# Performance work log

Hardware: AMD Instinct MI355X
Metric: run time of the kernel (lower is better)

## Reference

```python
import jax, jax.numpy as jnp
import numpy as np

B, N, K, F, L, H, ZMAX = 16, 1024, 16, 128, 4, 128, 100


def setup_inputs() -> dict:
    key = jax.random.key(0)
    ks = jax.random.split(key, 12)
    cell = jnp.eye(3, dtype=jnp.float32)[None] * 8.0 + 0.05 * jax.random.normal(ks[0], (B, 3, 3), dtype=jnp.float32)
    x = jax.random.uniform(ks[1], (B, N, 3), dtype=jnp.float32)
    z = jax.random.randint(ks[2], (B, N), 0, ZMAX)
    struct_size = jnp.full((B,), N, dtype=jnp.int32)
    emb = 0.02 * jax.random.normal(ks[3], (ZMAX, F), dtype=jnp.float32)
    din = 2 * F + 1
    W1 = jax.random.normal(ks[4], (L, din, F), dtype=jnp.float32) / np.sqrt(din)
    b1 = jnp.zeros((L, F), dtype=jnp.float32)
    W2 = jax.random.normal(ks[5], (L, F, F), dtype=jnp.float32) / np.sqrt(F)
    b2 = jnp.zeros((L, F), dtype=jnp.float32)
    A1 = jax.random.normal(ks[6], (din, H), dtype=jnp.float32) / np.sqrt(din)
    a1 = jnp.zeros((H,), dtype=jnp.float32)
    A2 = jax.random.normal(ks[7], (H, 1), dtype=jnp.float32) / np.sqrt(H)
    a2 = jnp.zeros((1,), dtype=jnp.float32)
    return {"cell": cell, "x": x, "z": z, "struct_size": struct_size, "emb": emb,
            "W1": W1, "b1": b1, "W2": W2, "b2": b2, "A1": A1, "a1": a1, "A2": A2, "a2": a2}


def _periodic_knn(cell, frac, k):
    # frac: [B,N,3] fractional coords, cell: [B,3,3] lattice rows.
    b, n, _ = frac.shape
    g = jnp.arange(-1, 2, dtype=frac.dtype)
    shifts = jnp.stack(jnp.meshgrid(g, g, g, indexing="ij"), -1).reshape(-1, 3)  # [27,3]
    rel = frac[:, None, :, :] - frac[:, :, None, :]  # rel[b,i,j] = frac_j - frac_i, [B,N,N,3]

    def body(carry, si):
        bd2, bsi = carry
        s, i = si
        cart = jnp.einsum("bijd,bde->bije", rel + s, cell)
        d2 = jnp.sum(cart * cart, axis=-1)
        upd = d2 < bd2
        return (jnp.where(upd, d2, bd2), jnp.where(upd, i, bsi)), None

    init = (jnp.full((b, n, n), 1e30, dtype=frac.dtype), jnp.zeros((b, n, n), dtype=jnp.int32))
    (d2min, simin), _ = jax.lax.scan(body, init, (shifts, jnp.arange(27, dtype=jnp.int32)))
    eye = jnp.eye(n, dtype=bool)
    d2min = jnp.where(eye[None], 1e30, d2min)  # exclude self (zero-shift) edges
    _, idx = jax.lax.top_k(-d2min, k)  # [B,N,k] neighbor indices
    sid = jnp.take_along_axis(simin, idx, axis=2)  # best image shift per edge
    svec = shifts[sid]  # [B,N,k,3]
    frac_j = jax.vmap(lambda f, i: f[i])(frac, idx)  # [B,N,k,3]
    vec = jnp.einsum("bnkd,bde->bnke", frac_j - frac[:, :, None, :] + svec, cell)
    d = jnp.sqrt(jnp.maximum(jnp.sum(vec * vec, axis=-1), 1e-12))  # [B,N,k]
    return idx, vec, d


def _edge_feat(h, idx, d):
    hj = jax.vmap(lambda hb, ib: hb[ib])(h, idx)  # [B,N,k,F]
    hi = jnp.broadcast_to(h[:, :, None, :], hj.shape)
    return jnp.concatenate([hi, hj, d[..., None]], axis=-1)  # [B,N,k,2F+1]


def reference(cell, x, z, struct_size, emb, W1, b1, W2, b2, A1, a1, A2, a2):
    frac = jnp.mod(x, 1.0)
    idx, vec, d = _periodic_knn(cell, frac, K)
    h = emb[z]  # [B,N,F]
    for l in range(W1.shape[0]):
        feat = _edge_feat(h, idx, d)
        m = jax.nn.silu(feat @ W1[l] + b1[l]) @ W2[l] + b2[l]  # [B,N,k,F]
        h = h + jnp.mean(m, axis=2)
    feat = _edge_feat(h, idx, d)
    w = jax.nn.silu(feat @ A1 + a1) @ A2 + a2  # [B,N,k,1]
    delta_cart = jnp.sum(w * vec, axis=2)  # [B,N,3]
    delta_frac = jnp.einsum("bnd,bde->bne", delta_cart, jnp.linalg.inv(cell))
    return x + delta_frac
```

## Files before the change

### kernel.cpp

```cpp
#include <hip/hip_runtime.h>

#define B_ 16
#define N_ 1024
#define K_ 16
#define F_ 128
#define L_ 4
#define DIN_ 257

typedef __bf16 bf16x8 __attribute__((ext_vector_type(8)));
typedef float f32x4 __attribute__((ext_vector_type(4)));

__device__ __forceinline__ float silu_f(float x) {
    return x / (1.0f + __expf(-x));
}

__device__ __forceinline__ unsigned short f2bf_bits(float f) {
    unsigned u = __builtin_bit_cast(unsigned, f);
    return (unsigned short)((u + 0x7FFFu + ((u >> 16) & 1u)) >> 16);
}

__global__ __launch_bounds__(256) void k_embed(const int* __restrict__ z,
                                               const float* __restrict__ emb,
                                               float* __restrict__ h,
                                               unsigned short* __restrict__ hbf) {
    int t = blockIdx.x * 256 + threadIdx.x;
    int node = t >> 5;
    int f4 = (t & 31) << 2;
    if (node >= B_ * N_) return;
    int zi = z[node];
    float4 v = *reinterpret_cast<const float4*>(&emb[zi * F_ + f4]);
    *reinterpret_cast<float4*>(&h[node * F_ + f4]) = v;
    ushort4 pk;
    pk.x = f2bf_bits(v.x); pk.y = f2bf_bits(v.y);
    pk.z = f2bf_bits(v.z); pk.w = f2bf_bits(v.w);
    *reinterpret_cast<ushort4*>(&hbf[node * F_ + f4]) = pk;
}

__global__ __launch_bounds__(256) void k_wconv(const float* __restrict__ W1,
                                               const float* __restrict__ W2,
                                               const float* __restrict__ A1,
                                               unsigned short* __restrict__ Wt1,
                                               unsigned short* __restrict__ Wt2,
                                               unsigned short* __restrict__ At1) {
    int id = blockIdx.x * 256 + threadIdx.x;
    if (id < L_ * 256 * 128) {
        int k = id & 127, n = (id >> 7) & 255, l = id >> 15;
        float v = (n < 128) ? W1[(size_t)l * DIN_ * F_ + (size_t)k * F_ + n]
                            : W1[(size_t)l * DIN_ * F_ + (size_t)(128 + k) * F_ + (n - 128)];
        Wt1[id] = f2bf_bits(v);
        return;
    }
    id -= L_ * 256 * 128;
    if (id < L_ * 128 * 128) {
        int k = id & 127, n = (id >> 7) & 127, l = id >> 14;
        Wt2[id] = f2bf_bits(W2[(size_t)l * F_ * F_ + (size_t)k * F_ + n]);
        return;
    }
    id -= L_ * 128 * 128;
    if (id < 256 * 128) {
        int k = id & 127, n = id >> 7;
        float v = (n < 128) ? A1[(size_t)k * 128 + n]
                            : A1[(size_t)(128 + k) * 128 + (n - 128)];
        At1[id] = f2bf_bits(v);
    }
}

__global__ __launch_bounds__(256) void k_knn(const float* __restrict__ x,
                                             const float* __restrict__ cell,
                                             int* __restrict__ idx_o,
                                             float* __restrict__ vec_o,
                                             float* __restrict__ d_o) {
    __shared__ float fr[N_ * 3];
    int b = blockIdx.x >> 8;
    int ib = (blockIdx.x & 255) << 2;
    const float* xb = x + b * N_ * 3;
    for (int u = threadIdx.x; u < N_ * 3; u += 256) {
        float xv = xb[u];
        fr[u] = xv - floorf(xv);
    }
    __syncthreads();
    int wave = threadIdx.x >> 6;
    int lane = threadIdx.x & 63;
    int i = ib + wave;

    const float* cb = cell + b * 9;
    float c00 = cb[0], c01 = cb[1], c02 = cb[2];
    float c10 = cb[3], c11 = cb[4], c12 = cb[5];
    float c20 = cb[6], c21 = cb[7], c22 = cb[8];
    float fi0 = fr[i * 3 + 0], fi1 = fr[i * 3 + 1], fi2 = fr[i * 3 + 2];

    unsigned long long k[16];
#pragma unroll
    for (int t = 0; t < 16; ++t) {
        int j = t * 64 + lane;
        float r0 = fr[j * 3 + 0] - fi0;
        float r1 = fr[j * 3 + 1] - fi1;
        float r2 = fr[j * 3 + 2] - fi2;
        float s0f = (r0 > 0.f) ? -1.f : 0.f;
        float s1f = (r1 > 0.f) ? -1.f : 0.f;
        float s2f = (r2 > 0.f) ? -1.f : 0.f;
        int sid_base = ((r0 > 0.f) ? 0 : 9) + ((r1 > 0.f) ? 0 : 3) + ((r2 > 0.f) ? 0 : 1);
        float rx0 = r0 + s0f, rx1 = r0 + (s0f + 1.0f);
        float ry0 = r1 + s1f, ry1 = r1 + (s1f + 1.0f);
        float rz0 = r2 + s2f, rz1 = r2 + (s2f + 1.0f);
        float best = 3e38f;
        int bsid = 0;
#pragma unroll
        for (int cbo = 0; cbo < 8; ++cbo) {
            float rs0 = (cbo & 4) ? rx1 : rx0;
            float rs1 = (cbo & 2) ? ry1 : ry0;
            float rs2 = (cbo & 1) ? rz1 : rz0;
            float cx = fmaf(rs2, c20, fmaf(rs1, c10, rs0 * c00));
            float cy = fmaf(rs2, c21, fmaf(rs1, c11, rs0 * c01));
            float cz = fmaf(rs2, c22, fmaf(rs1, c12, rs0 * c02));
            float d2 = fmaf(cz, cz, fmaf(cy, cy, cx * cx));
            int sid = sid_base + ((cbo >> 2) & 1) * 9 + ((cbo >> 1) & 1) * 3 + (cbo & 1);
            if (d2 < best) { best = d2; bsid = sid; }
        }
        if (j == i) best = 3e38f;
        unsigned db = __builtin_bit_cast(unsigned, best);
        k[t] = ((unsigned long long)db << 32) | (unsigned)((j << 5) | bsid);
    }

#define CE_(a, b)                                              \
    {                                                          \
        unsigned long long x_ = k[a], y_ = k[b];               \
        bool s_ = y_ < x_;                                     \
        k[a] = s_ ? y_ : x_;                                   \
        k[b] = s_ ? x_ : y_;                                   \
    }
    CE_(0,1) CE_(2,3) CE_(4,5) CE_(6,7) CE_(8,9) CE_(10,11) CE_(12,13) CE_(14,15)
    CE_(0,2) CE_(1,3) CE_(4,6) CE_(5,7) CE_(8,10) CE_(9,11) CE_(12,14) CE_(13,15)
    CE_(1,2) CE_(5,6) CE_(9,10) CE_(13,14)
    CE_(0,4) CE_(1,5) CE_(2,6) CE_(3,7) CE_(8,12) CE_(9,13) CE_(10,14) CE_(11,15)
    CE_(2,4) CE_(3,5) CE_(10,12) CE_(11,13)
    CE_(1,2) CE_(3,4) CE_(5,6) CE_(9,10) CE_(11,12) CE_(13,14)
    CE_(0,8) CE_(1,9) CE_(2,10) CE_(3,11) CE_(4,12) CE_(5,13) CE_(6,14) CE_(7,15)
    CE_(4,8) CE_(5,9) CE_(6,10) CE_(7,11)
    CE_(2,4) CE_(3,5) CE_(6,8) CE_(7,9) CE_(10,12) CE_(11,13)
    CE_(1,2) CE_(3,4) CE_(5,6) CE_(7,8) CE_(9,10) CE_(11,12) CE_(13,14)
#undef CE_

    unsigned long long sel = 0;
    for (int r = 0; r < 16; ++r) {
        unsigned long long m = k[0];
#pragma unroll
        for (int off = 32; off >= 1; off >>= 1) {
            unsigned long long o = __shfl_xor(m, off);
            if (o < m) m = o;
        }
        if (k[0] == m) {
#pragma unroll
            for (int t = 0; t < 15; ++t) k[t] = k[t + 1];
            k[15] = ~0ull;
        }
        if (lane == r) sel = m;
    }

    if (lane < 16) {
        unsigned pk = (unsigned)sel;
        int j = pk >> 5, sid = pk & 31;
        int s0 = sid / 9 - 1, s1 = (sid / 3) % 3 - 1, s2 = sid % 3 - 1;
        float rs0 = (fr[j * 3 + 0] - fi0) + (float)s0;
        float rs1 = (fr[j * 3 + 1] - fi1) + (float)s1;
        float rs2 = (fr[j * 3 + 2] - fi2) + (float)s2;
        float vx = fmaf(rs2, c20, fmaf(rs1, c10, rs0 * c00));
        float vy = fmaf(rs2, c21, fmaf(rs1, c11, rs0 * c01));
        float vz = fmaf(rs2, c22, fmaf(rs1, c12, rs0 * c02));
        float d2 = fmaf(vz, vz, fmaf(vy, vy, vx * vx));
        float dd = sqrtf(fmaxf(d2, 1e-12f));
        int node = b * N_ + i;
        int eo = node * K_ + lane;
        idx_o[eo] = j;
        d_o[eo] = dd;
        vec_o[eo * 3 + 0] = vx;
        vec_o[eo * 3 + 1] = vy;
        vec_o[eo * 3 + 2] = vz;
    }
}

template <int LOG_NT>
__global__ __launch_bounds__(256) void k_wgemm(const unsigned short* __restrict__ A,
                                               const unsigned short* __restrict__ Bt,
                                               float* __restrict__ C, int ldc) {
    constexpr int NT = 1 << LOG_NT;
    int wave = threadIdx.x >> 6, lane = threadIdx.x & 63;
    int tile = blockIdx.x * 4 + wave;
    int mt = tile >> LOG_NT, nt = tile & (NT - 1);
    int fr16 = lane & 15, ko = lane >> 4;
    const unsigned short* Ap = A + (size_t)(mt * 32 + fr16) * 128 + ko * 8;
    const unsigned short* Bp = Bt + (size_t)(nt * 32 + fr16) * 128 + ko * 8;

    bf16x8 a0[4], a1[4], b0[4], b1[4];
#pragma unroll
    for (int ks = 0; ks < 4; ++ks) {
        a0[ks] = *reinterpret_cast<const bf16x8*>(Ap + ks * 32);
        a1[ks] = *reinterpret_cast<const bf16x8*>(Ap + 16 * 128 + ks * 32);
        b0[ks] = *reinterpret_cast<const bf16x8*>(Bp + ks * 32);
        b1[ks] = *reinterpret_cast<const bf16x8*>(Bp + 16 * 128 + ks * 32);
    }
    f32x4 acc00 = {0.f, 0.f, 0.f, 0.f}, acc01 = acc00, acc10 = acc00, acc11 = acc00;
#pragma unroll
    for (int ks = 0; ks < 4; ++ks) {
        acc00 = __builtin_amdgcn_mfma_f32_16x16x32_bf16(a0[ks], b0[ks], acc00, 0, 0, 0);
        acc01 = __builtin_amdgcn_mfma_f32_16x16x32_bf16(a0[ks], b1[ks], acc01, 0, 0, 0);
        acc10 = __builtin_amdgcn_mfma_f32_16x16x32_bf16(a1[ks], b0[ks], acc10, 0, 0, 0);
        acc11 = __builtin_amdgcn_mfma_f32_16x16x32_bf16(a1[ks], b1[ks], acc11, 0, 0, 0);
    }
    int mrow = mt * 32 + ko * 4;
    int cbase = nt * 32 + fr16;
#define EPI_(FM, FN, ACC)                                                    \
    {                                                                        \
        int cc = cbase + FN * 16;                                            \
        _Pragma("unroll") for (int r = 0; r < 4; ++r) {                      \
            int row = mrow + FM * 16 + r;                                    \
            C[(size_t)row * ldc + cc] = ACC[r];                              \
        }                                                                    \
    }
    EPI_(0, 0, acc00) EPI_(0, 1, acc01) EPI_(1, 0, acc10) EPI_(1, 1, acc11)
#undef EPI_
}

__global__ __launch_bounds__(256) void k_layer(const float* __restrict__ UVin,
                                               const int* __restrict__ idx,
                                               const float* __restrict__ nd,
                                               const float* __restrict__ w1d,
                                               const float* __restrict__ b1l,
                                               const unsigned short* __restrict__ W2t,
                                               const float* __restrict__ b2l,
                                               float* __restrict__ h,
                                               const unsigned short* __restrict__ W1n,
                                               float* __restrict__ UVout) {
    __shared__ unsigned short svl[32][136];
    __shared__ unsigned short hbl[32][136];
    __shared__ int ilds[512];
    __shared__ float dlds[512];
    int tid = threadIdx.x;
    int gb = blockIdx.x;
    int batch = (gb & 7) + 8 * (gb >> 8);
    int ib = (gb >> 3) & 31;
    int node0 = batch * N_ + ib * 32;
    int bbase = batch * N_;

    ilds[tid] = idx[node0 * K_ + tid];
    ilds[tid + 256] = idx[node0 * K_ + tid + 256];
    dlds[tid] = nd[node0 * K_ + tid];
    dlds[tid + 256] = nd[node0 * K_ + tid + 256];
    __syncthreads();

#pragma unroll
    for (int it = 0; it < 2; ++it) {
        int tsk = it * 256 + tid;
        int gn = tsk >> 4, fc = tsk & 15, f0 = fc << 3;
        int node = node0 + gn;
        float u[8], wd[8], bb[8], acc[8];
#pragma unroll
        for (int q = 0; q < 8; q += 4) {
            float4 t = *reinterpret_cast<const float4*>(&UVin[(size_t)node * 256 + f0 + q]);
            u[q] = t.x; u[q + 1] = t.y; u[q + 2] = t.z; u[q + 3] = t.w;
            float4 t2 = *reinterpret_cast<const float4*>(&w1d[f0 + q]);
            wd[q] = t2.x; wd[q + 1] = t2.y; wd[q + 2] = t2.z; wd[q + 3] = t2.w;
            float4 t3 = *reinterpret_cast<const float4*>(&b1l[f0 + q]);
            bb[q] = t3.x; bb[q + 1] = t3.y; bb[q + 2] = t3.z; bb[q + 3] = t3.w;
        }
#pragma unroll
        for (int q = 0; q < 8; ++q) acc[q] = 0.f;
        for (int e = 0; e < K_; ++e) {
            int j = ilds[gn * K_ + e];
            float dd = dlds[gn * K_ + e];
            const float* vp = &UVin[(size_t)(bbase + j) * 256 + 128 + f0];
#pragma unroll
            for (int q = 0; q < 8; q += 4) {
                float4 t = *reinterpret_cast<const float4*>(&vp[q]);
                float v4[4] = {t.x, t.y, t.z, t.w};
#pragma unroll
                for (int w = 0; w < 4; ++w) {
                    float pre = u[q + w] + v4[w] + fmaf(dd, wd[q + w], bb[q + w]);
                    acc[q + w] += silu_f(pre);
                }
            }
        }
        const float inv_k = 1.0f / (float)K_;
        unsigned ow[4];
#pragma unroll
        for (int q = 0; q < 4; ++q)
            ow[q] = (unsigned)f2bf_bits(acc[2 * q] * inv_k) |
                    ((unsigned)f2bf_bits(acc[2 * q + 1] * inv_k) << 16);
        *reinterpret_cast<int4*>(&svl[gn][f0]) = make_int4(ow[0], ow[1], ow[2], ow[3]);
    }
    __syncthreads();

    int wave = tid >> 6, lane = tid & 63;
    int fr16 = lane & 15, ko = lane >> 4;

    {
        const unsigned short* Bp = W2t + (size_t)(wave * 32 + fr16) * 128 + ko * 8;
        bf16x8 a0[4], a1[4], b0[4], b1f[4];
#pragma unroll
        for (int ks = 0; ks < 4; ++ks) {
            a0[ks] = *reinterpret_cast<const bf16x8*>(&svl[fr16][ks * 32 + ko * 8]);
            a1[ks] = *reinterpret_cast<const bf16x8*>(&svl[fr16 + 16][ks * 32 + ko * 8]);
            b0[ks] = *reinterpret_cast<const bf16x8*>(Bp + ks * 32);
            b1f[ks] = *reinterpret_cast<const bf16x8*>(Bp + 16 * 128 + ks * 32);
        }
        f32x4 acc00 = {0.f, 0.f, 0.f, 0.f}, acc01 = acc00, acc10 = acc00, acc11 = acc00;
#pragma unroll
        for (int ks = 0; ks < 4; ++ks) {
            acc00 = __builtin_amdgcn_mfma_f32_16x16x32_bf16(a0[ks], b0[ks], acc00, 0, 0, 0);
            acc01 = __builtin_amdgcn_mfma_f32_16x16x32_bf16(a0[ks], b1f[ks], acc01, 0, 0, 0);
            acc10 = __builtin_amdgcn_mfma_f32_16x16x32_bf16(a1[ks], b0[ks], acc10, 0, 0, 0);
            acc11 = __builtin_amdgcn_mfma_f32_16x16x32_bf16(a1[ks], b1f[ks], acc11, 0, 0, 0);
        }
        int mrow = ko * 4;
        int cb0 = wave * 32 + fr16;
#define EPI2_(FM, FN, ACC)                                                     \
    {                                                                          \
        int col = cb0 + FN * 16;                                               \
        float bv = b2l[col];                                                   \
        _Pragma("unroll") for (int r = 0; r < 4; ++r) {                        \
            int row = mrow + FM * 16 + r;                                      \
            int grow = node0 + row;                                            \
            float val = ACC[r] + bv + h[(size_t)grow * 128 + col];             \
            h[(size_t)grow * 128 + col] = val;                                 \
            hbl[row][col] = f2bf_bits(val);                                    \
        }                                                                      \
    }
        EPI2_(0, 0, acc00) EPI2_(0, 1, acc01) EPI2_(1, 0, acc10) EPI2_(1, 1, acc11)
#undef EPI2_
    }
    __syncthreads();

#pragma unroll
    for (int half = 0; half < 2; ++half) {
        int nt = wave + half * 4;
        const unsigned short* Bp = W1n + (size_t)(nt * 32 + fr16) * 128 + ko * 8;
        bf16x8 a0[4], a1[4], b0[4], b1f[4];
#pragma unroll
        for (int ks = 0; ks < 4; ++ks) {
            a0[ks] = *reinterpret_cast<const bf16x8*>(&hbl[fr16][ks * 32 + ko * 8]);
            a1[ks] = *reinterpret_cast<const bf16x8*>(&hbl[fr16 + 16][ks * 32 + ko * 8]);
            b0[ks] = *reinterpret_cast<const bf16x8*>(Bp + ks * 32);
            b1f[ks] = *reinterpret_cast<const bf16x8*>(Bp + 16 * 128 + ks * 32);
        }
        f32x4 acc00 = {0.f, 0.f, 0.f, 0.f}, acc01 = acc00, acc10 = acc00, acc11 = acc00;
#pragma unroll
        for (int ks = 0; ks < 4; ++ks) {
            acc00 = __builtin_amdgcn_mfma_f32_16x16x32_bf16(a0[ks], b0[ks], acc00, 0, 0, 0);
            acc01 = __builtin_amdgcn_mfma_f32_16x16x32_bf16(a0[ks], b1f[ks], acc01, 0, 0, 0);
            acc10 = __builtin_amdgcn_mfma_f32_16x16x32_bf16(a1[ks], b0[ks], acc10, 0, 0, 0);
            acc11 = __builtin_amdgcn_mfma_f32_16x16x32_bf16(a1[ks], b1f[ks], acc11, 0, 0, 0);
        }
        int mrow = ko * 4;
        int cb0 = nt * 32 + fr16;
#define EPI1_(FM, FN, ACC)                                                     \
    {                                                                          \
        int col = cb0 + FN * 16;                                               \
        _Pragma("unroll") for (int r = 0; r < 4; ++r) {                        \
            int row = mrow + FM * 16 + r;                                      \
            UVout[(size_t)(node0 + row) * 256 + col] = ACC[r];                 \
        }                                                                      \
    }
        EPI1_(0, 0, acc00) EPI1_(0, 1, acc01) EPI1_(1, 0, acc10) EPI1_(1, 1, acc11)
#undef EPI1_
    }
}

__global__ __launch_bounds__(256) void k_final(const float* __restrict__ P,
                                               const int* __restrict__ idx,
                                               const float* __restrict__ nd,
                                               const float* __restrict__ nvec,
                                               const float* __restrict__ A1d,
                                               const float* __restrict__ a1v,
                                               const float* __restrict__ A2v,
                                               const float* __restrict__ a2v,
                                               const float* __restrict__ x,
                                               const float* __restrict__ cell,
                                               float* __restrict__ out) {
    __shared__ float plds[16][256];
    __shared__ float wlds[16][17];
    __shared__ float dclds[16][3];
    int gb = blockIdx.x;
    int batch = (gb & 7) + 8 * (gb >> 9);
    int ib = (gb >> 3) & 63;
    int node0 = batch * N_ + ib * 16;
    int g = threadIdx.x >> 4, fc = threadIdx.x & 15;
    int node = node0 + g;
    int b = node >> 10;
    int f0 = fc * 8;
    float pa[8], ad[8], aa[8], a2r[8];
#pragma unroll
    for (int q = 0; q < 8; q += 4) {
        float4 t = *reinterpret_cast<const float4*>(&P[(size_t)node * 256 + f0 + q]);
        pa[q] = t.x; pa[q + 1] = t.y; pa[q + 2] = t.z; pa[q + 3] = t.w;
        float4 t2 = *reinterpret_cast<const float4*>(&A1d[f0 + q]);
        ad[q] = t2.x; ad[q + 1] = t2.y; ad[q + 2] = t2.z; ad[q + 3] = t2.w;
        float4 t3 = *reinterpret_cast<const float4*>(&a1v[f0 + q]);
        aa[q] = t3.x; aa[q + 1] = t3.y; aa[q + 2] = t3.z; aa[q + 3] = t3.w;
        float4 t4 = *reinterpret_cast<const float4*>(&A2v[f0 + q]);
        a2r[q] = t4.x; a2r[q + 1] = t4.y; a2r[q + 2] = t4.z; a2r[q + 3] = t4.w;
    }
    int ebase = node * K_;
    for (int e = 0; e < K_; ++e) {
        int j = idx[ebase + e];
        float dd = nd[ebase + e];
        const float* vp = &P[(size_t)(b * N_ + j) * 256 + 128 + f0];
        float part = 0.f;
#pragma unroll
        for (int q = 0; q < 8; q += 4) {
            float4 t = *reinterpret_cast<const float4*>(&vp[q]);
            float v4[4] = {t.x, t.y, t.z, t.w};
#pragma unroll
            for (int w = 0; w < 4; ++w) {
                float pre = pa[q + w] + v4[w] + fmaf(dd, ad[q + w], aa[q + w]);
                part = fmaf(silu_f(pre), a2r[q + w], part);
            }
        }
        plds[e][(g << 4) | fc] = part;
    }
    __syncthreads();
    {
        int g2 = threadIdx.x >> 4, e2 = threadIdx.x & 15;
        float w = a2v[0];
#pragma unroll
        for (int f2 = 0; f2 < 16; ++f2) w += plds[e2][(g2 << 4) | f2];
        wlds[g2][e2] = w;
    }
    __syncthreads();
    if (threadIdx.x < 48) {
        int gg = threadIdx.x & 15, c = threadIdx.x >> 4;
        int noded = node0 + gg;
        float dc = 0.f;
#pragma unroll
        for (int e = 0; e < K_; ++e)
            dc = fmaf(wlds[gg][e], nvec[(size_t)(noded * K_ + e) * 3 + c], dc);
        dclds[gg][c] = dc;
    }
    __syncthreads();
    if (threadIdx.x < 48) {
        int gg = threadIdx.x & 15, c = threadIdx.x >> 4;
        int noded = node0 + gg;
        int bb2 = noded >> 10;
        const float* cb = cell + bb2 * 9;
        float c00 = cb[0], c01 = cb[1], c02 = cb[2];
        float c10 = cb[3], c11 = cb[4], c12 = cb[5];
        float c20 = cb[6], c21 = cb[7], c22 = cb[8];
        float det = c00 * (c11 * c22 - c12 * c21) - c01 * (c10 * c22 - c12 * c20) +
                    c02 * (c10 * c21 - c11 * c20);
        float rdet = 1.0f / det;
        float i0c, i1c, i2c;
        if (c == 0) {
            i0c = (c11 * c22 - c12 * c21) * rdet;
            i1c = -(c10 * c22 - c12 * c20) * rdet;
            i2c = (c10 * c21 - c11 * c20) * rdet;
        } else if (c == 1) {
            i0c = -(c01 * c22 - c02 * c21) * rdet;
            i1c = (c00 * c22 - c02 * c20) * rdet;
            i2c = -(c00 * c21 - c01 * c20) * rdet;
        } else {
            i0c = (c01 * c12 - c02 * c11) * rdet;
            i1c = -(c00 * c12 - c02 * c10) * rdet;
            i2c = (c00 * c11 - c01 * c10) * rdet;
        }
        float df = dclds[gg][0] * i0c + dclds[gg][1] * i1c + dclds[gg][2] * i2c;
        out[(size_t)noded * 3 + c] = x[(size_t)noded * 3 + c] + df;
    }
}

extern "C" void kernel_launch(void* const* d_in, const int* in_sizes, int n_in,
                              void* d_out, int out_size, void* d_ws, size_t ws_size,
                              hipStream_t stream) {
    (void)in_sizes; (void)n_in; (void)out_size; (void)ws_size;
    const float* cell = (const float*)d_in[0];
    const float* x    = (const float*)d_in[1];
    const int*   z    = (const int*)d_in[2];
    const float* emb  = (const float*)d_in[4];
    const float* W1   = (const float*)d_in[5];
    const float* b1   = (const float*)d_in[6];
    const float* W2   = (const float*)d_in[7];
    const float* b2   = (const float*)d_in[8];
    const float* A1   = (const float*)d_in[9];
    const float* a1   = (const float*)d_in[10];
    const float* A2   = (const float*)d_in[11];
    const float* a2   = (const float*)d_in[12];
    float* out = (float*)d_out;

    char* ws = (char*)d_ws;
    size_t off = 0;
    auto alloc = [&](size_t bytes) {
        void* p = ws + off;
        off = (off + bytes + 255) & ~(size_t)255;
        return p;
    };
    int* idx    = (int*)alloc((size_t)B_ * N_ * K_ * 4);
    float* nd   = (float*)alloc((size_t)B_ * N_ * K_ * 4);
    float* nvec = (float*)alloc((size_t)B_ * N_ * K_ * 3 * 4);
    float* h0   = (float*)alloc((size_t)B_ * N_ * F_ * 4);
    float* uv0  = (float*)alloc((size_t)B_ * N_ * 256 * 4);
    float* uv1  = (float*)alloc((size_t)B_ * N_ * 256 * 4);
    unsigned short* hbf = (unsigned short*)alloc((size_t)B_ * N_ * F_ * 2);
    unsigned short* Wt1 = (unsigned short*)alloc((size_t)L_ * 256 * 128 * 2);
    unsigned short* Wt2 = (unsigned short*)alloc((size_t)L_ * 128 * 128 * 2);
    unsigned short* At1 = (unsigned short*)alloc((size_t)256 * 128 * 2);

    int conv_total = L_ * 256 * 128 + L_ * 128 * 128 + 256 * 128;
    k_wconv<<<(conv_total + 255) / 256, 256, 0, stream>>>(W1, W2, A1, Wt1, Wt2, At1);
    k_embed<<<2048, 256, 0, stream>>>(z, emb, h0, hbf);
    k_knn<<<4096, 256, 0, stream>>>(x, cell, idx, nvec, nd);

    k_wgemm<3><<<1024, 256, 0, stream>>>(hbf, Wt1, uv0, 256);

    for (int l = 0; l < L_; ++l) {
        const float* uin = (l & 1) ? uv1 : uv0;
        float* uout = (l & 1) ? uv0 : uv1;
        const unsigned short* W1next = (l < 3) ? (Wt1 + (size_t)(l + 1) * 256 * 128) : At1;
        k_layer<<<512, 256, 0, stream>>>(uin, idx, nd,
                                         W1 + (size_t)l * DIN_ * F_ + 256 * F_, b1 + l * F_,
                                         Wt2 + (size_t)l * 128 * 128, b2 + l * F_, h0,
                                         W1next, uout);
    }
    k_final<<<1024, 256, 0, stream>>>(uv0, idx, nd, nvec, A1 + 256 * F_, a1, A2, a2, x, cell,
                                      out);
}
```

Baseline: 270.2 us.

## Fuse all stages into one persistent cooperative megakernel with grid syncs

Replaces the sequence of separate launches (weight conversion, embedding, kNN, first GEMM, four layers, final) with a single cooperative kernel that runs each stage in turn, separated by grid-wide barriers. The grid is sized from occupancy, and the old multi-launch path stays as a fallback. The aim is to remove per-launch overhead and inter-kernel gaps. In exchange, the grid is capped at resident blocks, which can reduce parallelism in stages like kNN that previously used 4096 blocks, and grid.sync adds its own barrier cost.

```diff
diff --git a/kernel.cpp b/kernel.cpp
--- a/kernel.cpp
+++ b/kernel.cpp
@@ -1,4 +1,7 @@
 #include <hip/hip_runtime.h>
+#include <hip/hip_cooperative_groups.h>
+
+namespace cg = cooperative_groups;
 
 #define B_ 16
 #define N_ 1024
@@ -17,6 +20,445 @@
 __device__ __forceinline__ unsigned short f2bf_bits(float f) {
     unsigned u = __builtin_bit_cast(unsigned, f);
     return (unsigned short)((u + 0x7FFFu + ((u >> 16) & 1u)) >> 16);
+}
+
+__global__ __launch_bounds__(256, 4) void k_mega(
+    const float* __restrict__ cell, const float* __restrict__ x,
+    const int* __restrict__ z, const float* __restrict__ emb,
+    const float* __restrict__ W1, const float* __restrict__ b1,
+    const float* __restrict__ W2, const float* __restrict__ b2,
+    const float* __restrict__ A1, const float* __restrict__ a1,
+    const float* __restrict__ A2, const float* __restrict__ a2,
+    float* __restrict__ out,
+    int* __restrict__ idx, float* __restrict__ nd, float* __restrict__ nvec,
+    float* __restrict__ h0, float* __restrict__ uv0, float* __restrict__ uv1,
+    unsigned short* __restrict__ hbf, unsigned short* __restrict__ Wt1,
+    unsigned short* __restrict__ Wt2, unsigned short* __restrict__ At1) {
+    cg::grid_group grid = cg::this_grid();
+    __shared__ __align__(16) char smem[17664];
+    int tid = threadIdx.x;
+    int gb = blockIdx.x;
+    int nb = gridDim.x;
+    int gid = gb * 256 + tid;
+    int stride = nb * 256;
+    int wave = tid >> 6, lane = tid & 63;
+    int fr16 = lane & 15, ko = lane >> 4;
+
+    {
+        const int conv_total = L_ * 256 * 128 + L_ * 128 * 128 + 256 * 128;
+        for (int id0 = gid; id0 < conv_total; id0 += stride) {
+            int id = id0;
+            if (id < L_ * 256 * 128) {
+                int k = id & 127, n = (id >> 7) & 255, l = id >> 15;
+                float v = (n < 128)
+                              ? W1[(size_t)l * DIN_ * F_ + (size_t)k * F_ + n]
+                              : W1[(size_t)l * DIN_ * F_ + (size_t)(128 + k) * F_ + (n - 128)];
+                Wt1[id] = f2bf_bits(v);
+            } else {
+                int id2 = id - L_ * 256 * 128;
+                if (id2 < L_ * 128 * 128) {
+                    int k = id2 & 127, n = (id2 >> 7) & 127, l = id2 >> 14;
+                    Wt2[id2] = f2bf_bits(W2[(size_t)l * F_ * F_ + (size_t)k * F_ + n]);
+                } else {
+                    int id3 = id2 - L_ * 128 * 128;
+                    int k = id3 & 127, n = id3 >> 7;
+                    float v = (n < 128) ? A1[(size_t)k * 128 + n]
+                                        : A1[(size_t)(128 + k) * 128 + (n - 128)];
+                    At1[id3] = f2bf_bits(v);
+                }
+            }
+        }
+        for (int t = gid; t < B_ * N_ * 32; t += stride) {
+            int node = t >> 5;
+            int f4 = (t & 31) << 2;
+            int zi = z[node];
+            float4 v = *reinterpret_cast<const float4*>(&emb[zi * F_ + f4]);
+            *reinterpret_cast<float4*>(&h0[node * F_ + f4]) = v;
+            ushort4 pk;
+            pk.x = f2bf_bits(v.x); pk.y = f2bf_bits(v.y);
+            pk.z = f2bf_bits(v.z); pk.w = f2bf_bits(v.w);
+            *reinterpret_cast<ushort4*>(&hbf[node * F_ + f4]) = pk;
+        }
+    }
+    __threadfence();
+    grid.sync();
+
+    {
+        float* fr = (float*)smem;
+        for (int c = gb; c < 1024; c += nb) {
+            int batch = ((c & 7) << 1) | ((c >> 3) & 1);
+            int ib = c >> 4;
+            __syncthreads();
+            const float* xb = x + batch * N_ * 3;
+            for (int u = tid; u < N_ * 3; u += 256) {
+                float xv = xb[u];
+                fr[u] = xv - floorf(xv);
+            }
+            __syncthreads();
+            const float* cb = cell + batch * 9;
+            float c00 = cb[0], c01 = cb[1], c02 = cb[2];
+            float c10 = cb[3], c11 = cb[4], c12 = cb[5];
+            float c20 = cb[6], c21 = cb[7], c22 = cb[8];
+
+            for (int r4 = 0; r4 < 4; ++r4) {
+                int i = ib * 16 + wave * 4 + r4;
+                float fi0 = fr[i * 3 + 0], fi1 = fr[i * 3 + 1], fi2 = fr[i * 3 + 2];
+
+                unsigned long long k[16];
+#pragma unroll
+                for (int t = 0; t < 16; ++t) {
+                    int j = t * 64 + lane;
+                    float r0 = fr[j * 3 + 0] - fi0;
+                    float r1 = fr[j * 3 + 1] - fi1;
+                    float r2 = fr[j * 3 + 2] - fi2;
+                    float s0f = (r0 > 0.f) ? -1.f : 0.f;
+                    float s1f = (r1 > 0.f) ? -1.f : 0.f;
+                    float s2f = (r2 > 0.f) ? -1.f : 0.f;
+                    int sid_base = ((r0 > 0.f) ? 0 : 9) + ((r1 > 0.f) ? 0 : 3) + ((r2 > 0.f) ? 0 : 1);
+                    float rx0 = r0 + s0f, rx1 = r0 + (s0f + 1.0f);
+                    float ry0 = r1 + s1f, ry1 = r1 + (s1f + 1.0f);
+                    float rz0 = r2 + s2f, rz1 = r2 + (s2f + 1.0f);
+                    float best = 3e38f;
+                    int bsid = 0;
+#pragma unroll
+                    for (int cbo = 0; cbo < 8; ++cbo) {
+                        float rs0 = (cbo & 4) ? rx1 : rx0;
+                        float rs1 = (cbo & 2) ? ry1 : ry0;
+                        float rs2 = (cbo & 1) ? rz1 : rz0;
+                        float cx = fmaf(rs2, c20, fmaf(rs1, c10, rs0 * c00));
+                        float cy = fmaf(rs2, c21, fmaf(rs1, c11, rs0 * c01));
+                        float cz = fmaf(rs2, c22, fmaf(rs1, c12, rs0 * c02));
+                        float d2 = fmaf(cz, cz, fmaf(cy, cy, cx * cx));
+                        int sid = sid_base + ((cbo >> 2) & 1) * 9 + ((cbo >> 1) & 1) * 3 + (cbo & 1);
+                        if (d2 < best) { best = d2; bsid = sid; }
+                    }
+                    if (j == i) best = 3e38f;
+                    unsigned db = __builtin_bit_cast(unsigned, best);
+                    k[t] = ((unsigned long long)db << 32) | (unsigned)((j << 5) | bsid);
+                }
+
+#define CE_(a, b)                                              \
+    {                                                          \
+        unsigned long long x_ = k[a], y_ = k[b];               \
+        bool s_ = y_ < x_;                                     \
+        k[a] = s_ ? y_ : x_;                                   \
+        k[b] = s_ ? x_ : y_;                                   \
+    }
+                CE_(0,1) CE_(2,3) CE_(4,5) CE_(6,7) CE_(8,9) CE_(10,11) CE_(12,13) CE_(14,15)
+                CE_(0,2) CE_(1,3) CE_(4,6) CE_(5,7) CE_(8,10) CE_(9,11) CE_(12,14) CE_(13,15)
+                CE_(1,2) CE_(5,6) CE_(9,10) CE_(13,14)
+                CE_(0,4) CE_(1,5) CE_(2,6) CE_(3,7) CE_(8,12) CE_(9,13) CE_(10,14) CE_(11,15)
+                CE_(2,4) CE_(3,5) CE_(10,12) CE_(11,13)
+                CE_(1,2) CE_(3,4) CE_(5,6) CE_(9,10) CE_(11,12) CE_(13,14)
+                CE_(0,8) CE_(1,9) CE_(2,10) CE_(3,11) CE_(4,12) CE_(5,13) CE_(6,14) CE_(7,15)
+                CE_(4,8) CE_(5,9) CE_(6,10) CE_(7,11)
+                CE_(2,4) CE_(3,5) CE_(6,8) CE_(7,9) CE_(10,12) CE_(11,13)
+                CE_(1,2) CE_(3,4) CE_(5,6) CE_(7,8) CE_(9,10) CE_(11,12) CE_(13,14)
+#undef CE_
+
+                unsigned long long sel = 0;
+                for (int r = 0; r < 16; ++r) {
+                    unsigned long long m = k[0];
+#pragma unroll
+                    for (int off = 32; off >= 1; off >>= 1) {
+                        unsigned long long o = __shfl_xor(m, off);
+                        if (o < m) m = o;
+                    }
+                    if (k[0] == m) {
+#pragma unroll
+                        for (int t = 0; t < 15; ++t) k[t] = k[t + 1];
+                        k[15] = ~0ull;
+                    }
+                    if (lane == r) sel = m;
+                }
+
+                if (lane < 16) {
+                    unsigned pk = (unsigned)sel;
+                    int j = pk >> 5, sid = pk & 31;
+                    int s0 = sid / 9 - 1, s1 = (sid / 3) % 3 - 1, s2 = sid % 3 - 1;
+                    float rs0 = (fr[j * 3 + 0] - fi0) + (float)s0;
+                    float rs1 = (fr[j * 3 + 1] - fi1) + (float)s1;
+                    float rs2 = (fr[j * 3 + 2] - fi2) + (float)s2;
+                    float vx = fmaf(rs2, c20, fmaf(rs1, c10, rs0 * c00));
+                    float vy = fmaf(rs2, c21, fmaf(rs1, c11, rs0 * c01));
+                    float vz = fmaf(rs2, c22, fmaf(rs1, c12, rs0 * c02));
+                    float d2 = fmaf(vz, vz, fmaf(vy, vy, vx * vx));
+                    float dd = sqrtf(fmaxf(d2, 1e-12f));
+                    int node = batch * N_ + i;
+                    int eo = node * K_ + lane;
+                    idx[eo] = j;
+                    nd[eo] = dd;
+                    nvec[eo * 3 + 0] = vx;
+                    nvec[eo * 3 + 1] = vy;
+                    nvec[eo * 3 + 2] = vz;
+                }
+            }
+        }
+
+        for (int t = gb * 4 + wave; t < 4096; t += nb * 4) {
+            int mt = t >> 3, nt = t & 7;
+            const unsigned short* Ap = hbf + (size_t)(mt * 32 + fr16) * 128 + ko * 8;
+            const unsigned short* Bp = Wt1 + (size_t)(nt * 32 + fr16) * 128 + ko * 8;
+            bf16x8 a0[4], a1v_[4], b0[4], b1v_[4];
+#pragma unroll
+            for (int ks = 0; ks < 4; ++ks) {
+                a0[ks] = *reinterpret_cast<const bf16x8*>(Ap + ks * 32);
+                a1v_[ks] = *reinterpret_cast<const bf16x8*>(Ap + 16 * 128 + ks * 32);
+                b0[ks] = *reinterpret_cast<const bf16x8*>(Bp + ks * 32);
+                b1v_[ks] = *reinterpret_cast<const bf16x8*>(Bp + 16 * 128 + ks * 32);
+            }
+            f32x4 acc00 = {0.f, 0.f, 0.f, 0.f}, acc01 = acc00, acc10 = acc00, acc11 = acc00;
+#pragma unroll
+            for (int ks = 0; ks < 4; ++ks) {
+                acc00 = __builtin_amdgcn_mfma_f32_16x16x32_bf16(a0[ks], b0[ks], acc00, 0, 0, 0);
+                acc01 = __builtin_amdgcn_mfma_f32_16x16x32_bf16(a0[ks], b1v_[ks], acc01, 0, 0, 0);
+                acc10 = __builtin_amdgcn_mfma_f32_16x16x32_bf16(a1v_[ks], b0[ks], acc10, 0, 0, 0);
+                acc11 = __builtin_amdgcn_mfma_f32_16x16x32_bf16(a1v_[ks], b1v_[ks], acc11, 0, 0, 0);
+            }
+            int mrow = mt * 32 + ko * 4;
+            int cbase = nt * 32 + fr16;
+#define EPI_(FM, FN, ACC)                                                    \
+    {                                                                        \
+        int cc = cbase + FN * 16;                                            \
+        _Pragma("unroll") for (int r = 0; r < 4; ++r) {                      \
+            int row = mrow + FM * 16 + r;                                    \
+            uv0[(size_t)row * 256 + cc] = ACC[r];                            \
+        }                                                                    \
+    }
+            EPI_(0, 0, acc00) EPI_(0, 1, acc01) EPI_(1, 0, acc10) EPI_(1, 1, acc11)
+#undef EPI_
+        }
+    }
+
+    {
+        unsigned short (*svl)[136] = (unsigned short (*)[136])smem;
+        unsigned short (*hbl)[136] = (unsigned short (*)[136])(smem + 4352);
+        int* ilds = (int*)(smem + 8704);
+        float* dlds = (float*)(smem + 9728);
+
+        for (int l = 0; l < L_; ++l) {
+            __threadfence();
+            grid.sync();
+            const float* UVin = (l & 1) ? uv1 : uv0;
+            float* UVout = (l & 1) ? uv0 : uv1;
+            const unsigned short* W1n = (l < 3) ? (Wt1 + (size_t)(l + 1) * 256 * 128) : At1;
+            const unsigned short* W2t = Wt2 + (size_t)l * 128 * 128;
+            const float* w1d = W1 + (size_t)l * DIN_ * F_ + 256 * F_;
+            const float* b1l = b1 + l * F_;
+            const float* b2l = b2 + l * F_;
+
+            for (int c = gb; c < 1024; c += nb) {
+                int batch = ((c & 7) << 1) | ((c >> 3) & 1);
+                int ib = c >> 4;
+                int node0 = batch * N_ + ib * 16;
+                int bbase = batch * N_;
+                __syncthreads();
+                ilds[tid] = idx[node0 * K_ + tid];
+                dlds[tid] = nd[node0 * K_ + tid];
+                __syncthreads();
+
+                {
+                    int gn = tid >> 4, fc = tid & 15, f0 = fc << 3;
+                    int node = node0 + gn;
+                    float u[8], wd[8], bb[8], acc[8];
+#pragma unroll
+                    for (int q = 0; q < 8; q += 4) {
+                        float4 t = *reinterpret_cast<const float4*>(&UVin[(size_t)node * 256 + f0 + q]);
+                        u[q] = t.x; u[q + 1] = t.y; u[q + 2] = t.z; u[q + 3] = t.w;
+                        float4 t2 = *reinterpret_cast<const float4*>(&w1d[f0 + q]);
+                        wd[q] = t2.x; wd[q + 1] = t2.y; wd[q + 2] = t2.z; wd[q + 3] = t2.w;
+                        float4 t3 = *reinterpret_cast<const float4*>(&b1l[f0 + q]);
+                        bb[q] = t3.x; bb[q + 1] = t3.y; bb[q + 2] = t3.z; bb[q + 3] = t3.w;
+                    }
+#pragma unroll
+                    for (int q = 0; q < 8; ++q) acc[q] = 0.f;
+                    for (int e = 0; e < K_; ++e) {
+                        int j = ilds[gn * K_ + e];
+                        float dd = dlds[gn * K_ + e];
+                        const float* vp = &UVin[(size_t)(bbase + j) * 256 + 128 + f0];
+#pragma unroll
+                        for (int q = 0; q < 8; q += 4) {
+                            float4 t = *reinterpret_cast<const float4*>(&vp[q]);
+                            float v4[4] = {t.x, t.y, t.z, t.w};
+#pragma unroll
+                            for (int w = 0; w < 4; ++w) {
+                                float pre = u[q + w] + v4[w] + fmaf(dd, wd[q + w], bb[q + w]);
+                                acc[q + w] += silu_f(pre);
+                            }
+                        }
+                    }
+                    const float inv_k = 1.0f / (float)K_;
+                    unsigned ow[4];
+#pragma unroll
+                    for (int q = 0; q < 4; ++q)
+                        ow[q] = (unsigned)f2bf_bits(acc[2 * q] * inv_k) |
+                                ((unsigned)f2bf_bits(acc[2 * q + 1] * inv_k) << 16);
+                    *reinterpret_cast<int4*>(&svl[gn][f0]) = make_int4(ow[0], ow[1], ow[2], ow[3]);
+                }
+                __syncthreads();
+
+                {
+                    const unsigned short* Bp = W2t + (size_t)(wave * 32 + fr16) * 128 + ko * 8;
+                    bf16x8 a0[4], b0[4], b1f[4];
+#pragma unroll
+                    for (int ks = 0; ks < 4; ++ks) {
+                        a0[ks] = *reinterpret_cast<const bf16x8*>(&svl[fr16][ks * 32 + ko * 8]);
+                        b0[ks] = *reinterpret_cast<const bf16x8*>(Bp + ks * 32);
+                        b1f[ks] = *reinterpret_cast<const bf16x8*>(Bp + 16 * 128 + ks * 32);
+                    }
+                    f32x4 acc00 = {0.f, 0.f, 0.f, 0.f}, acc01 = acc00;
+#pragma unroll
+                    for (int ks = 0; ks < 4; ++ks) {
+                        acc00 = __builtin_amdgcn_mfma_f32_16x16x32_bf16(a0[ks], b0[ks], acc00, 0, 0, 0);
+                        acc01 = __builtin_amdgcn_mfma_f32_16x16x32_bf16(a0[ks], b1f[ks], acc01, 0, 0, 0);
+                    }
+                    int cb0 = wave * 32 + fr16;
+#define EPI2_(FN, ACC)                                                         \
+    {                                                                          \
+        int col = cb0 + FN * 16;                                               \
+        float bv = b2l[col];                                                   \
+        _Pragma("unroll") for (int r = 0; r < 4; ++r) {                        \
+            int row = ko * 4 + r;                                              \
+            int grow = node0 + row;                                            \
+            float val = ACC[r] + bv + h0[(size_t)grow * 128 + col];            \
+            h0[(size_t)grow * 128 + col] = val;                                \
+            hbl[row][col] = f2bf_bits(val);                                    \
+        }                                                                      \
+    }
+                    EPI2_(0, acc00) EPI2_(1, acc01)
+#undef EPI2_
+                }
+                __syncthreads();
+
+#pragma unroll
+                for (int half = 0; half < 2; ++half) {
+                    int nt2 = wave + half * 4;
+                    const unsigned short* Bp = W1n + (size_t)(nt2 * 32 + fr16) * 128 + ko * 8;
+                    bf16x8 a0[4], b0[4], b1f[4];
+#pragma unroll
+                    for (int ks = 0; ks < 4; ++ks) {
+                        a0[ks] = *reinterpret_cast<const bf16x8*>(&hbl[fr16][ks * 32 + ko * 8]);
+                        b0[ks] = *reinterpret_cast<const bf16x8*>(Bp + ks * 32);
+                        b1f[ks] = *reinterpret_cast<const bf16x8*>(Bp + 16 * 128 + ks * 32);
+                    }
+                    f32x4 acc00 = {0.f, 0.f, 0.f, 0.f}, acc01 = acc00;
+#pragma unroll
+                    for (int ks = 0; ks < 4; ++ks) {
+                        acc00 = __builtin_amdgcn_mfma_f32_16x16x32_bf16(a0[ks], b0[ks], acc00, 0, 0, 0);
+                        acc01 = __builtin_amdgcn_mfma_f32_16x16x32_bf16(a0[ks], b1f[ks], acc01, 0, 0, 0);
+                    }
+                    int cb0 = nt2 * 32 + fr16;
+#define EPI1_(FN, ACC)                                                         \
+    {                                                                          \
+        int col = cb0 + FN * 16;                                               \
+        _Pragma("unroll") for (int r = 0; r < 4; ++r) {                        \
+            int row = ko * 4 + r;                                              \
+            UVout[(size_t)(node0 + row) * 256 + col] = ACC[r];                 \
+        }                                                                      \
+    }
+                    EPI1_(0, acc00) EPI1_(1, acc01)
+#undef EPI1_
+                }
+            }
+        }
+    }
+
+    __threadfence();
+    grid.sync();
+
+    {
+        float (*plds)[256] = (float (*)[256])smem;
+        float (*wlds)[17] = (float (*)[17])(smem + 16384);
+        float (*dclds)[3] = (float (*)[3])(smem + 17472);
+        const float* P = uv0;
+        const float* A1d = A1 + 256 * F_;
+        for (int c = gb; c < 1024; c += nb) {
+            int batch = ((c & 7) << 1) | ((c >> 3) & 1);
+            int ib = c >> 4;
+            int node0 = batch * N_ + ib * 16;
+            int bbase = batch * N_;
+            __syncthreads();
+            int g = tid >> 4, fc = tid & 15;
+            int node = node0 + g;
+            int f0 = fc * 8;
+            float pa[8], ad[8], aa[8], a2r[8];
+#pragma unroll
+            for (int q = 0; q < 8; q += 4) {
+                float4 t = *reinterpret_cast<const float4*>(&P[(size_t)node * 256 + f0 + q]);
+                pa[q] = t.x; pa[q + 1] = t.y; pa[q + 2] = t.z; pa[q + 3] = t.w;
+                float4 t2 = *reinterpret_cast<const float4*>(&A1d[f0 + q]);
+                ad[q] = t2.x; ad[q + 1] = t2.y; ad[q + 2] = t2.z; ad[q + 3] = t2.w;
+                float4 t3 = *reinterpret_cast<const float4*>(&a1[f0 + q]);
+                aa[q] = t3.x; aa[q + 1] = t3.y; aa[q + 2] = t3.z; aa[q + 3] = t3.w;
+                float4 t4 = *reinterpret_cast<const float4*>(&A2[f0 + q]);
+                a2r[q] = t4.x; a2r[q + 1] = t4.y; a2r[q + 2] = t4.z; a2r[q + 3] = t4.w;
+            }
+            int ebase = node * K_;
+            for (int e = 0; e < K_; ++e) {
+                int j = idx[ebase + e];
+                float dd = nd[ebase + e];
+                const float* vp = &P[(size_t)(bbase + j) * 256 + 128 + f0];
+                float part = 0.f;
+#pragma unroll
+                for (int q = 0; q < 8; q += 4) {
+                    float4 t = *reinterpret_cast<const float4*>(&vp[q]);
+                    float v4[4] = {t.x, t.y, t.z, t.w};
+#pragma unroll
+                    for (int w = 0; w < 4; ++w) {
+                        float pre = pa[q + w] + v4[w] + fmaf(dd, ad[q + w], aa[q + w]);
+                        part = fmaf(silu_f(pre), a2r[q + w], part);
+                    }
+                }
+                plds[e][(g << 4) | fc] = part;
+            }
+            __syncthreads();
+            {
+                int g2 = tid >> 4, e2 = tid & 15;
+                float w = a2[0];
+#pragma unroll
+                for (int f2 = 0; f2 < 16; ++f2) w += plds[e2][(g2 << 4) | f2];
+                wlds[g2][e2] = w;
+            }
+            __syncthreads();
+            if (tid < 48) {
+                int gg = tid & 15, cc = tid >> 4;
+                int noded = node0 + gg;
+                float dc = 0.f;
+#pragma unroll
+                for (int e = 0; e < K_; ++e)
+                    dc = fmaf(wlds[gg][e], nvec[(size_t)(noded * K_ + e) * 3 + cc], dc);
+                dclds[gg][cc] = dc;
+            }
+            __syncthreads();
+            if (tid < 48) {
+                int gg = tid & 15, cc = tid >> 4;
+                int noded = node0 + gg;
+                const float* cb = cell + batch * 9;
+                float c00 = cb[0], c01 = cb[1], c02 = cb[2];
+                float c10 = cb[3], c11 = cb[4], c12 = cb[5];
+                float c20 = cb[6], c21 = cb[7], c22 = cb[8];
+                float det = c00 * (c11 * c22 - c12 * c21) - c01 * (c10 * c22 - c12 * c20) +
+                            c02 * (c10 * c21 - c11 * c20);
+                float rdet = 1.0f / det;
+                float i0c, i1c, i2c;
+                if (cc == 0) {
+                    i0c = (c11 * c22 - c12 * c21) * rdet;
+                    i1c = -(c10 * c22 - c12 * c20) * rdet;
+                    i2c = (c10 * c21 - c11 * c20) * rdet;
+                } else if (cc == 1) {
+                    i0c = -(c01 * c22 - c02 * c21) * rdet;
+                    i1c = (c00 * c22 - c02 * c20) * rdet;
+                    i2c = -(c00 * c21 - c01 * c20) * rdet;
+                } else {
+                    i0c = (c01 * c12 - c02 * c11) * rdet;
+                    i1c = -(c00 * c12 - c02 * c10) * rdet;
+                    i2c = (c00 * c11 - c01 * c10) * rdet;
+                }
+                float df = dclds[gg][0] * i0c + dclds[gg][1] * i1c + dclds[gg][2] * i2c;
+                out[(size_t)noded * 3 + cc] = x[(size_t)noded * 3 + cc] + df;
+            }
+        }
+    }
 }
 
 __global__ __launch_bounds__(256) void k_embed(const int* __restrict__ z,
@@ -502,13 +944,36 @@
     unsigned short* Wt2 = (unsigned short*)alloc((size_t)L_ * 128 * 128 * 2);
     unsigned short* At1 = (unsigned short*)alloc((size_t)256 * 128 * 2);
 
+    int dev = 0;
+    (void)hipGetDevice(&dev);
+    int numCU = 0;
+    (void)hipDeviceGetAttribute(&numCU, hipDeviceAttributeMultiprocessorCount, dev);
+    int maxB = 0;
+    (void)hipOccupancyMaxActiveBlocksPerMultiprocessor(
+        &maxB, reinterpret_cast<const void*>(&k_mega), 256, 0);
+    long long cap = (long long)maxB * (long long)numCU;
+    int gridn = (int)(cap > 1024 ? 1024 : cap);
+
+    if (gridn >= 64) {
+        void* args[] = {
+            (void*)&cell, (void*)&x, (void*)&z, (void*)&emb,
+            (void*)&W1, (void*)&b1, (void*)&W2, (void*)&b2,
+            (void*)&A1, (void*)&a1, (void*)&A2, (void*)&a2,
+            (void*)&out,
+            (void*)&idx, (void*)&nd, (void*)&nvec, (void*)&h0,
+            (void*)&uv0, (void*)&uv1, (void*)&hbf, (void*)&Wt1,
+            (void*)&Wt2, (void*)&At1,
+        };
+        hipError_t e = hipLaunchCooperativeKernel(
+            reinterpret_cast<const void*>(&k_mega), dim3(gridn), dim3(256), args, 0, stream);
+        if (e == hipSuccess) return;
+    }
+
     int conv_total = L_ * 256 * 128 + L_ * 128 * 128 + 256 * 128;
     k_wconv<<<(conv_total + 255) / 256, 256, 0, stream>>>(W1, W2, A1, Wt1, Wt2, At1);
     k_embed<<<2048, 256, 0, stream>>>(z, emb, h0, hbf);
     k_knn<<<4096, 256, 0, stream>>>(x, cell, idx, nvec, nd);
-
     k_wgemm<3><<<1024, 256, 0, stream>>>(hbf, Wt1, uv0, 256);
-
     for (int l = 0; l < L_; ++l) {
         const float* uin = (l & 1) ? uv1 : uv0;
         float* uout = (l & 1) ? uv0 : uv1;
```

New measurement: 1.018 ms. 3.77x slower.
